# Kernel optimization log

Measured on AMD Instinct MI355X. Metric: run time of the kernel, lower is better.

## Reference

```python
import jax, jax.numpy as jnp
import numpy as np

LN_EPS = 1e-5

def _layernorm(x, g, b):
    mu = jnp.mean(x, axis=-1, keepdims=True)
    var = jnp.var(x, axis=-1, keepdims=True)
    return (x - mu) * jax.lax.rsqrt(var + LN_EPS) * g + b

def setup_inputs() -> dict:
    key = jax.random.key(0)
    ks = jax.random.split(key, 8)
    B, L, d_atom, d_hid = 8, 128, 256, 32
    return {
        "z":    jax.random.normal(ks[0], (B, L, d_atom), dtype=jnp.float32),
        "W_in": jax.random.normal(ks[1], (d_atom, 2 * d_hid), dtype=jnp.float32) * 0.02,
        "b_in": jnp.zeros((2 * d_hid,), dtype=jnp.float32),
        "ln_g": jnp.ones((2 * d_hid,), dtype=jnp.float32),
        "ln_b": jnp.zeros((2 * d_hid,), dtype=jnp.float32),
        "W1":   jax.random.normal(ks[2], (d_hid * d_hid, 21), dtype=jnp.float32) * 0.02,
        "b1":   jnp.zeros((21,), dtype=jnp.float32),
        "W2":   jax.random.normal(ks[3], (d_hid * d_hid, 30), dtype=jnp.float32) * 0.02,
        "b2":   jnp.zeros((30,), dtype=jnp.float32),
    }

def reference(z, W_in, b_in, ln_g, ln_b, W1, b1, W2, b2):
    # linear_in: Linear -> exact GELU -> LayerNorm
    ab = _layernorm(jax.nn.gelu(z @ W_in + b_in, approximate=False), ln_g, ln_b)
    h = ab.shape[-1] // 2
    a, b = ab[..., :h], ab[..., h:]              # (B, L, h) each
    # Fused bilinear form: outer(a_l, b_m) flattened to h*h, then Linear.
    # Equivalent to materializing (B, L, L, h*h) and matmul, reassociated.
    W1r = W1.reshape(h, h, -1)                   # (h, h, 21)
    W2r = W2.reshape(h, h, -1)                   # (h, h, 30)
    x1 = jnp.einsum('blc,bmd,cdk->blmk', a, b, W1r) + b1  # (B, L, L, 21)
    x2 = jnp.einsum('blc,bmd,cdk->blmk', a, b, W2r) + b2  # (B, L, L, 30)
    return (x1, x2)
```

## Files before the change

### kernel.cpp

```cpp
#include <hip/hip_runtime.h>
#include <hip/hip_bf16.h>
#include <math.h>

#define NB 8
#define NL 128
#define D_ATOM 256
#define DH 32
#define DAB 64
#define K1 21
#define K2 30
#define KT 51
#define ROWS (NB*NL)
#define LN_EPS 1e-5f

#define OUT1_ROW (NL*K1)
#define OUT2_ROW (NL*K2)
#define STAGE_N  (OUT1_ROW + OUT2_ROW)
#define WCAT 1632

typedef __attribute__((ext_vector_type(8))) short bf16x8;
typedef __attribute__((ext_vector_type(4))) float f32x4;

__device__ __forceinline__ unsigned short f2bf(float x) {
    __hip_bfloat16 h = __float2bfloat16(x);
    return *reinterpret_cast<unsigned short*>(&h);
}

__global__ __launch_bounds__(256) void ln_wprep_kernel(
    const float* __restrict__ z, const float* __restrict__ W_in,
    const float* __restrict__ b_in, const float* __restrict__ ln_g,
    const float* __restrict__ ln_b, const float* __restrict__ W1,
    const float* __restrict__ W2, float* __restrict__ a_ws,
    unsigned short* __restrict__ bbf, unsigned short* __restrict__ Wlin2)
{
    const int t = threadIdx.x;

    if (blockIdx.x >= 256) {
        const int base = ((int)blockIdx.x - 256) * 512;
        #pragma unroll
        for (int e = 0; e < 2; ++e) {
            int p  = base + e * 256 + t;
            int c  = p >> 8, t2 = p & 255;
            unsigned short v[8];
            #pragma unroll
            for (int s = 0; s < 8; ++s) {
                int o = s * 256 + t2;
                float val = 0.f;
                if (o < 672)       val = W1[c * 672 + o];
                else if (o < WCAT) val = W2[c * 960 + (o - 672)];
                v[s] = f2bf(val);
            }
            uint4 wq;
            wq.x = (unsigned)v[0] | ((unsigned)v[1] << 16);
            wq.y = (unsigned)v[2] | ((unsigned)v[3] << 16);
            wq.z = (unsigned)v[4] | ((unsigned)v[5] << 16);
            wq.w = (unsigned)v[6] | ((unsigned)v[7] << 16);
            ((uint4*)Wlin2)[p] = wq;
        }
        return;
    }

    __shared__ float Wl[D_ATOM * DAB];
    __shared__ float zl[4][D_ATOM];
    const int w = t >> 6, j = t & 63;
    const int row0 = blockIdx.x * 4;

    #pragma unroll
    for (int s = 0; s < 16; ++s) {
        int i4 = t + s * 256;
        ((float4*)Wl)[i4] = ((const float4*)W_in)[i4];
    }
    ((float4*)zl)[t] = ((const float4*)(z + (size_t)row0 * D_ATOM))[t];
    __syncthreads();

    float acc = b_in[j];
    #pragma unroll 8
    for (int i = 0; i < D_ATOM; ++i)
        acc = fmaf(zl[w][i], Wl[i * DAB + j], acc);

    float g = 0.5f * acc * (1.0f + erff(acc * 0.70710678118654752f));

    float s = g, sq = g * g;
    #pragma unroll
    for (int msk = 1; msk < 64; msk <<= 1) {
        s  += __shfl_xor(s,  msk, 64);
        sq += __shfl_xor(sq, msk, 64);
    }
    float mu  = s  * (1.0f / 64.0f);
    float var = sq * (1.0f / 64.0f) - mu * mu;
    float y = (g - mu) * rsqrtf(var + LN_EPS) * ln_g[j] + ln_b[j];

    const int row = row0 + w;
    if (j < DH) {
        a_ws[row * DH + j] = y;
    } else {
        const int d = j - DH, m = row & 127, batch = row >> 7;
        bbf[batch * 4096 + ((m >> 4) << 9) +
            ((((m & 15) | ((d >> 3) << 4)) << 3) | (d & 7))] = f2bf(y);
    }
}

__global__ __launch_bounds__(256, 4) void pair_kernel(
    const float* __restrict__ a_ws, const unsigned short* __restrict__ bbf,
    const unsigned short* __restrict__ Wlin2, const float* __restrict__ b1v,
    const float* __restrict__ b2v, float* __restrict__ out)
{
    const int row0  = blockIdx.x * 2;
    const int batch = row0 >> 7;
    const int t     = threadIdx.x;
    const int w  = t >> 6, l = t & 63;
    const int lg = l >> 4, li = l & 15;

    __shared__ unsigned short Tf[2 * 4 * 64 * 8];
    __shared__ __align__(16) float stg[STAGE_N];
    __shared__ float al[2][DH];

    #pragma unroll
    for (int s = 0; s < 8; ++s)
        ((unsigned int*)Tf)[t + s * 256] = 0u;
    if (t < 2 * DH) al[t >> 5][t & 31] = a_ws[row0 * DH + t];
    __syncthreads();

    {
        float tacc0[7], tacc1[7];
        int fidx[7];
        bool val[7];
        #pragma unroll
        for (int s = 0; s < 7; ++s) {
            int o = t + s * 256;
            val[s] = (o < WCAT);
            int oo = val[s] ? o : 0;
            int d, k;
            if (oo < 672) { d = oo / 21; k = oo % 21; }
            else { int o2 = oo - 672; d = o2 / 30; k = 21 + o2 % 30; }
            fidx[s] = (((k >> 4) * 64 + ((k & 15) | ((d >> 3) << 4))) << 3) | (d & 7);
            tacc0[s] = 0.f; tacc1[s] = 0.f;
        }
        const uint4* wbase = ((const uint4*)Wlin2) + t;
        #pragma unroll 4
        for (int c = 0; c < DH; ++c) {
            float ac0 = al[0][c], ac1 = al[1][c];
            uint4 wq = wbase[c * 256];
            float wv[7];
            wv[0] = __uint_as_float(wq.x << 16);
            wv[1] = __uint_as_float(wq.x & 0xffff0000u);
            wv[2] = __uint_as_float(wq.y << 16);
            wv[3] = __uint_as_float(wq.y & 0xffff0000u);
            wv[4] = __uint_as_float(wq.z << 16);
            wv[5] = __uint_as_float(wq.z & 0xffff0000u);
            wv[6] = __uint_as_float(wq.w << 16);
            #pragma unroll
            for (int s = 0; s < 7; ++s) {
                tacc0[s] = fmaf(ac0, wv[s], tacc0[s]);
                tacc1[s] = fmaf(ac1, wv[s], tacc1[s]);
            }
        }
        #pragma unroll
        for (int s = 0; s < 7; ++s) {
            if (val[s]) {
                Tf[fidx[s]]        = f2bf(tacc0[s]);
                Tf[2048 + fidx[s]] = f2bf(tacc1[s]);
            }
        }
    }
    __syncthreads();

    const int r  = w >> 1;
    const int mh = w & 1;

    bf16x8 afr[4], bfr[4];
    #pragma unroll
    for (int i = 0; i < 4; ++i)
        afr[i] = ((const bf16x8*)bbf)[batch * 512 + (mh * 4 + i) * 64 + l];
    #pragma unroll
    for (int kt = 0; kt < 4; ++kt)
        bfr[kt] = ((const bf16x8*)Tf)[(r * 4 + kt) * 64 + l];

    float bias[4];
    #pragma unroll
    for (int kt = 0; kt < 4; ++kt) {
        int k = kt * 16 + li;
        bias[kt] = (k < K1) ? b1v[k] : (k < KT ? b2v[k - K1] : 0.f);
    }

    #pragma unroll
    for (int rr = 0; rr < 2; ++rr) {
        if (r == rr) {
            #pragma unroll
            for (int i = 0; i < 4; ++i) {
                const int mbase = (mh * 4 + i) * 16 + lg * 4;
                #pragma unroll
                for (int kt = 0; kt < 4; ++kt) {
                    f32x4 acc = __builtin_amdgcn_mfma_f32_16x16x32_bf16(
                        afr[i], bfr[kt], (f32x4){0.f, 0.f, 0.f, 0.f}, 0, 0, 0);
                    const int k = kt * 16 + li;
                    if (k < K1) {
                        #pragma unroll
                        for (int q = 0; q < 4; ++q)
                            stg[(mbase + q) * K1 + k] = acc[q] + bias[kt];
                    } else if (k < KT) {
                        #pragma unroll
                        for (int q = 0; q < 4; ++q)
                            stg[OUT1_ROW + (mbase + q) * K2 + (k - K1)] = acc[q] + bias[kt];
                    }
                }
            }
        }
        __syncthreads();

        const int row = row0 + rr;
        float* o1 = out + (size_t)row * OUT1_ROW;
        float* o2 = out + (size_t)ROWS * OUT1_ROW + (size_t)row * OUT2_ROW;
        const float4* s1 = (const float4*)stg;
        const float4* s2 = (const float4*)(stg + OUT1_ROW);
        for (int i4 = t; i4 < OUT1_ROW / 4; i4 += 256)
            ((float4*)o1)[i4] = s1[i4];
        for (int i4 = t; i4 < OUT2_ROW / 4; i4 += 256)
            ((float4*)o2)[i4] = s2[i4];
        if (rr == 0) __syncthreads();
    }
}

extern "C" void kernel_launch(void* const* d_in, const int* in_sizes, int n_in,
                              void* d_out, int out_size, void* d_ws, size_t ws_size,
                              hipStream_t stream) {
    const float* z    = (const float*)d_in[0];
    const float* W_in = (const float*)d_in[1];
    const float* b_in = (const float*)d_in[2];
    const float* ln_g = (const float*)d_in[3];
    const float* ln_b = (const float*)d_in[4];
    const float* W1   = (const float*)d_in[5];
    const float* b1   = (const float*)d_in[6];
    const float* W2   = (const float*)d_in[7];
    const float* b2   = (const float*)d_in[8];
    float* out = (float*)d_out;

    float*          a_ws  = (float*)d_ws;
    unsigned short* bbf   = (unsigned short*)(a_ws + 32768);
    unsigned short* Wlin2 = bbf + 32768;

    ln_wprep_kernel<<<272, 256, 0, stream>>>(z, W_in, b_in, ln_g, ln_b,
                                             W1, W2, a_ws, bbf, Wlin2);
    pair_kernel<<<ROWS / 2, 256, 0, stream>>>(a_ws, bbf, Wlin2, b1, b2, out);
}
```

Before: 22.68 us.

## Drop LDS staging of W_in in LN kernel; use 64-thread blocks, two rows per wave

```diff
diff --git a/kernel.cpp b/kernel.cpp
--- a/kernel.cpp
+++ b/kernel.cpp
@@ -26,7 +26,7 @@
     return *reinterpret_cast<unsigned short*>(&h);
 }
 
-__global__ __launch_bounds__(256) void ln_wprep_kernel(
+__global__ __launch_bounds__(64) void ln_wprep_kernel(
     const float* __restrict__ z, const float* __restrict__ W_in,
     const float* __restrict__ b_in, const float* __restrict__ ln_g,
     const float* __restrict__ ln_b, const float* __restrict__ W1,
@@ -35,11 +35,11 @@
 {
     const int t = threadIdx.x;
 
-    if (blockIdx.x >= 256) {
-        const int base = ((int)blockIdx.x - 256) * 512;
+    if (blockIdx.x >= 512) {
+        const int base = ((int)blockIdx.x - 512) * 128;
         #pragma unroll
         for (int e = 0; e < 2; ++e) {
-            int p  = base + e * 256 + t;
+            int p  = base + e * 64 + t;
             int c  = p >> 8, t2 = p & 255;
             unsigned short v[8];
             #pragma unroll
@@ -60,43 +60,49 @@
         return;
     }
 
-    __shared__ float Wl[D_ATOM * DAB];
-    __shared__ float zl[4][D_ATOM];
-    const int w = t >> 6, j = t & 63;
-    const int row0 = blockIdx.x * 4;
-
-    #pragma unroll
-    for (int s = 0; s < 16; ++s) {
-        int i4 = t + s * 256;
-        ((float4*)Wl)[i4] = ((const float4*)W_in)[i4];
-    }
-    ((float4*)zl)[t] = ((const float4*)(z + (size_t)row0 * D_ATOM))[t];
-    __syncthreads();
-
-    float acc = b_in[j];
+    const int r0 = blockIdx.x * 2;
+    const int j  = t;
+    const float* z0 = z + (size_t)r0 * D_ATOM;
+    const float* z1 = z0 + D_ATOM;
+
+    float acc0 = b_in[j], acc1 = acc0;
     #pragma unroll 8
-    for (int i = 0; i < D_ATOM; ++i)
-        acc = fmaf(zl[w][i], Wl[i * DAB + j], acc);
-
-    float g = 0.5f * acc * (1.0f + erff(acc * 0.70710678118654752f));
-
-    float s = g, sq = g * g;
+    for (int c = 0; c < D_ATOM; ++c) {
+        float wv = W_in[c * DAB + j];
+        acc0 = fmaf(z0[c], wv, acc0);
+        acc1 = fmaf(z1[c], wv, acc1);
+    }
+
+    float g0 = 0.5f * acc0 * (1.0f + erff(acc0 * 0.70710678118654752f));
+    float g1 = 0.5f * acc1 * (1.0f + erff(acc1 * 0.70710678118654752f));
+
+    float s0 = g0, sq0 = g0 * g0, s1 = g1, sq1 = g1 * g1;
     #pragma unroll
     for (int msk = 1; msk < 64; msk <<= 1) {
-        s  += __shfl_xor(s,  msk, 64);
-        sq += __shfl_xor(sq, msk, 64);
-    }
-    float mu  = s  * (1.0f / 64.0f);
-    float var = sq * (1.0f / 64.0f) - mu * mu;
-    float y = (g - mu) * rsqrtf(var + LN_EPS) * ln_g[j] + ln_b[j];
-
-    const int row = row0 + w;
-    if (j < DH) {
-        a_ws[row * DH + j] = y;
-    } else {
-        const int d = j - DH, m = row & 127, batch = row >> 7;
-        bbf[batch * 4096 + ((m >> 4) << 9) +
-            ((((m & 15) | ((d >> 3) << 4)) << 3) | (d & 7))] = f2bf(y);
+        s0  += __shfl_xor(s0,  msk, 64);
+        sq0 += __shfl_xor(sq0, msk, 64);
+        s1  += __shfl_xor(s1,  msk, 64);
+        sq1 += __shfl_xor(sq1, msk, 64);
+    }
+    float mu0  = s0  * (1.0f / 64.0f);
+    float var0 = sq0 * (1.0f / 64.0f) - mu0 * mu0;
+    float mu1  = s1  * (1.0f / 64.0f);
+    float var1 = sq1 * (1.0f / 64.0f) - mu1 * mu1;
+    float gg = ln_g[j], bb = ln_b[j];
+    float y0 = (g0 - mu0) * rsqrtf(var0 + LN_EPS) * gg + bb;
+    float y1 = (g1 - mu1) * rsqrtf(var1 + LN_EPS) * gg + bb;
+
+    #pragma unroll
+    for (int rr = 0; rr < 2; ++rr) {
+        const int row = r0 + rr;
+        float y = rr ? y1 : y0;
+        if (j < DH) {
+            a_ws[row * DH + j] = y;
+        } else {
+            const int d = j - DH, m = row & 127, batch = row >> 7;
+            bbf[batch * 4096 + ((m >> 4) << 9) +
+                ((((m & 15) | ((d >> 3) << 4)) << 3) | (d & 7))] = f2bf(y);
+        }
     }
 }
 
@@ -239,7 +245,7 @@
     unsigned short* bbf   = (unsigned short*)(a_ws + 32768);
     unsigned short* Wlin2 = bbf + 32768;
 
-    ln_wprep_kernel<<<272, 256, 0, stream>>>(z, W_in, b_in, ln_g, ln_b,
-                                             W1, W2, a_ws, bbf, Wlin2);
+    ln_wprep_kernel<<<576, 64, 0, stream>>>(z, W_in, b_in, ln_g, ln_b,
+                                            W1, W2, a_ws, bbf, Wlin2);
     pair_kernel<<<ROWS / 2, 256, 0, stream>>>(a_ws, bbf, Wlin2, b1, b2, out);
 }
```

After: 26.80 us. +18.2%, slower.

## Write pair outputs directly to global and fold weight prep into LN blocks

Applied to the files above, without the earlier changes.

```diff
diff --git a/kernel.cpp b/kernel.cpp
--- a/kernel.cpp
+++ b/kernel.cpp
@@ -15,7 +15,6 @@
 
 #define OUT1_ROW (NL*K1)
 #define OUT2_ROW (NL*K2)
-#define STAGE_N  (OUT1_ROW + OUT2_ROW)
 #define WCAT 1632
 
 typedef __attribute__((ext_vector_type(8))) short bf16x8;
@@ -33,35 +32,9 @@
     const float* __restrict__ W2, float* __restrict__ a_ws,
     unsigned short* __restrict__ bbf, unsigned short* __restrict__ Wlin2)
 {
-    const int t = threadIdx.x;
-
-    if (blockIdx.x >= 256) {
-        const int base = ((int)blockIdx.x - 256) * 512;
-        #pragma unroll
-        for (int e = 0; e < 2; ++e) {
-            int p  = base + e * 256 + t;
-            int c  = p >> 8, t2 = p & 255;
-            unsigned short v[8];
-            #pragma unroll
-            for (int s = 0; s < 8; ++s) {
-                int o = s * 256 + t2;
-                float val = 0.f;
-                if (o < 672)       val = W1[c * 672 + o];
-                else if (o < WCAT) val = W2[c * 960 + (o - 672)];
-                v[s] = f2bf(val);
-            }
-            uint4 wq;
-            wq.x = (unsigned)v[0] | ((unsigned)v[1] << 16);
-            wq.y = (unsigned)v[2] | ((unsigned)v[3] << 16);
-            wq.z = (unsigned)v[4] | ((unsigned)v[5] << 16);
-            wq.w = (unsigned)v[6] | ((unsigned)v[7] << 16);
-            ((uint4*)Wlin2)[p] = wq;
-        }
-        return;
-    }
-
     __shared__ float Wl[D_ATOM * DAB];
     __shared__ float zl[4][D_ATOM];
+    const int t = threadIdx.x;
     const int w = t >> 6, j = t & 63;
     const int row0 = blockIdx.x * 4;
 
@@ -97,6 +70,26 @@
         const int d = j - DH, m = row & 127, batch = row >> 7;
         bbf[batch * 4096 + ((m >> 4) << 9) +
             ((((m & 15) | ((d >> 3) << 4)) << 3) | (d & 7))] = f2bf(y);
+    }
+
+    if (t < 32) {
+        int p  = (int)blockIdx.x * 32 + t;
+        int c  = p >> 8, t2 = p & 255;
+        unsigned short v[8];
+        #pragma unroll
+        for (int s2 = 0; s2 < 8; ++s2) {
+            int o = s2 * 256 + t2;
+            float val = 0.f;
+            if (o < 672)       val = W1[c * 672 + o];
+            else if (o < WCAT) val = W2[c * 960 + (o - 672)];
+            v[s2] = f2bf(val);
+        }
+        uint4 wq;
+        wq.x = (unsigned)v[0] | ((unsigned)v[1] << 16);
+        wq.y = (unsigned)v[2] | ((unsigned)v[3] << 16);
+        wq.z = (unsigned)v[4] | ((unsigned)v[5] << 16);
+        wq.w = (unsigned)v[6] | ((unsigned)v[7] << 16);
+        ((uint4*)Wlin2)[p] = wq;
     }
 }
 
@@ -112,7 +105,6 @@
     const int lg = l >> 4, li = l & 15;
 
     __shared__ unsigned short Tf[2 * 4 * 64 * 8];
-    __shared__ __align__(16) float stg[STAGE_N];
     __shared__ float al[2][DH];
 
     #pragma unroll
@@ -183,41 +175,28 @@
         bias[kt] = (k < K1) ? b1v[k] : (k < KT ? b2v[k - K1] : 0.f);
     }
 
-    #pragma unroll
-    for (int rr = 0; rr < 2; ++rr) {
-        if (r == rr) {
-            #pragma unroll
-            for (int i = 0; i < 4; ++i) {
-                const int mbase = (mh * 4 + i) * 16 + lg * 4;
+    const int row = row0 + r;
+    float* o1 = out + (size_t)row * OUT1_ROW;
+    float* o2 = out + (size_t)ROWS * OUT1_ROW + (size_t)row * OUT2_ROW;
+
+    #pragma unroll
+    for (int i = 0; i < 4; ++i) {
+        const int mbase = (mh * 4 + i) * 16 + lg * 4;
+        #pragma unroll
+        for (int kt = 0; kt < 4; ++kt) {
+            f32x4 acc = __builtin_amdgcn_mfma_f32_16x16x32_bf16(
+                afr[i], bfr[kt], (f32x4){0.f, 0.f, 0.f, 0.f}, 0, 0, 0);
+            const int k = kt * 16 + li;
+            if (k < K1) {
                 #pragma unroll
-                for (int kt = 0; kt < 4; ++kt) {
-                    f32x4 acc = __builtin_amdgcn_mfma_f32_16x16x32_bf16(
-                        afr[i], bfr[kt], (f32x4){0.f, 0.f, 0.f, 0.f}, 0, 0, 0);
-                    const int k = kt * 16 + li;
-                    if (k < K1) {
-                        #pragma unroll
-                        for (int q = 0; q < 4; ++q)
-                            stg[(mbase + q) * K1 + k] = acc[q] + bias[kt];
-                    } else if (k < KT) {
-                        #pragma unroll
-                        for (int q = 0; q < 4; ++q)
-                            stg[OUT1_ROW + (mbase + q) * K2 + (k - K1)] = acc[q] + bias[kt];
-                    }
-                }
+                for (int q = 0; q < 4; ++q)
+                    o1[(mbase + q) * K1 + k] = acc[q] + bias[kt];
+            } else if (k < KT) {
+                #pragma unroll
+                for (int q = 0; q < 4; ++q)
+                    o2[(mbase + q) * K2 + (k - K1)] = acc[q] + bias[kt];
             }
         }
-        __syncthreads();
-
-        const int row = row0 + rr;
-        float* o1 = out + (size_t)row * OUT1_ROW;
-        float* o2 = out + (size_t)ROWS * OUT1_ROW + (size_t)row * OUT2_ROW;
-        const float4* s1 = (const float4*)stg;
-        const float4* s2 = (const float4*)(stg + OUT1_ROW);
-        for (int i4 = t; i4 < OUT1_ROW / 4; i4 += 256)
-            ((float4*)o1)[i4] = s1[i4];
-        for (int i4 = t; i4 < OUT2_ROW / 4; i4 += 256)
-            ((float4*)o2)[i4] = s2[i4];
-        if (rr == 0) __syncthreads();
     }
 }
 
@@ -239,7 +218,7 @@
     unsigned short* bbf   = (unsigned short*)(a_ws + 32768);
     unsigned short* Wlin2 = bbf + 32768;
 
-    ln_wprep_kernel<<<272, 256, 0, stream>>>(z, W_in, b_in, ln_g, ln_b,
+    ln_wprep_kernel<<<256, 256, 0, stream>>>(z, W_in, b_in, ln_g, ln_b,
                                              W1, W2, a_ws, bbf, Wlin2);
     pair_kernel<<<ROWS / 2, 256, 0, stream>>>(a_ws, bbf, Wlin2, b1, b2, out);
 }
```

Result: slower. 24.32 us (+7.2%).
